# Kernel tuning notes

Measured on AMD Instinct MI355X. Metric: run time of the kernel, lower is better.

## Reference

```python
import jax, jax.numpy as jnp
import numpy as np

K_SIZE = 3
STRIDE = 1
PAD = 1


def _extract_patches(X, k, stride, pad):
    """X: [N,H,W,C] -> patches [N,Ho,Wo,k*k*C], ordered (dh, dw, c) to match
    filters.reshape(c_out, k*k*C)."""
    Xp = jnp.pad(X, ((0, 0), (pad, pad), (pad, pad), (0, 0)))
    N, Hp, Wp, C = Xp.shape
    Ho = (Hp - k) // stride + 1
    Wo = (Wp - k) // stride + 1
    slabs = [Xp[:, dh:dh + stride * Ho:stride, dw:dw + stride * Wo:stride, :]
             for dh in range(k) for dw in range(k)]  # fixed small k*k loop
    P = jnp.stack(slabs, axis=3)  # [N,Ho,Wo,k*k,C]
    return P.reshape(N, Ho, Wo, k * k * C)


def setup_inputs() -> dict:
    key = jax.random.key(0)
    k1, k2 = jax.random.split(key)
    X = jax.random.normal(k1, (8, 32, 32, 32), dtype=jnp.float32)
    filters = jax.random.normal(k2, (64, 3, 3, 32), dtype=jnp.float32)
    return {"X": X, "filters": filters}


def reference(X, filters):
    # AdderNet forward: Z[n,h,w,f] = sum_{dh,dw,c} |window(n,h,w) - filters[f]|
    c_out = filters.shape[0]
    P = _extract_patches(X, K_SIZE, STRIDE, PAD)  # [N,Ho,Wo,K]
    N, Ho, Wo, K = P.shape
    F = filters.reshape(c_out, K)
    # L1 distance between every patch and every filter: [M, c_out]
    D = jnp.abs(P.reshape(-1, 1, K) - F[None, :, :]).sum(axis=-1)
    return D.reshape(N, Ho, Wo, c_out)
```

## Files before the change

kernel.cpp:

```cpp
#include <hip/hip_runtime.h>


#define BLOCK 256

__global__ __launch_bounds__(256, 2) void adder_fwd(const float* __restrict__ X,
                                                    const float* __restrict__ Fg,
                                                    float* __restrict__ out) {
    __shared__ float Xs[4 * 34 * 36];

    const int b = blockIdx.x;
    const int fq = b & 3;
    const int hp = (b >> 2) & 15;
    const int n = b >> 6;
    const int h0 = hp * 2;
    const int tid = threadIdx.x;

    #pragma unroll
    for (int i = 0; i < 5; ++i) {
        int idx = tid + BLOCK * i;
        if (idx < 1088) {
            int c4 = idx & 7;
            int t  = idx >> 3;
            int wc = t % 34;
            int rr = t / 34;
            int hr = h0 + rr - 1;
            int gw = wc - 1;
            float4 v = make_float4(0.f, 0.f, 0.f, 0.f);
            if ((unsigned)hr < 32u && (unsigned)gw < 32u) {
                v = ((const float4*)(X + (((size_t)n * 32 + hr) * 32 + gw) * 32))[c4];
            }
            ((float4*)(Xs + (rr * 34 + wc) * 36))[c4] = v;
        }
    }
    __syncthreads();

    const int w    = tid & 31;
    const int hh   = (tid >> 5) & 1;
    const int wave = tid >> 6;
    const int f0   = fq * 16 + wave * 4;

    const float* fb = Fg + (size_t)f0 * 288;

    float a0 = 0.f, a1 = 0.f, a2 = 0.f, a3 = 0.f;

    #pragma unroll
    for (int r = 0; r < 3; ++r) {
        #pragma unroll
        for (int dw = 0; dw < 3; ++dw) {
            const float4* xp = (const float4*)(Xs + ((hh + r) * 34 + (w + dw)) * 36);
            const float*  ftap = fb + (r * 3 + dw) * 32;
            #pragma unroll
            for (int c4 = 0; c4 < 8; ++c4) {
                float4 xv = xp[c4];
                float4 f0v = ((const float4*)(ftap + 0 * 288))[c4];
                float4 f1v = ((const float4*)(ftap + 1 * 288))[c4];
                float4 f2v = ((const float4*)(ftap + 2 * 288))[c4];
                float4 f3v = ((const float4*)(ftap + 3 * 288))[c4];
                a0 += fabsf(xv.x - f0v.x) + fabsf(xv.y - f0v.y)
                    + fabsf(xv.z - f0v.z) + fabsf(xv.w - f0v.w);
                a1 += fabsf(xv.x - f1v.x) + fabsf(xv.y - f1v.y)
                    + fabsf(xv.z - f1v.z) + fabsf(xv.w - f1v.w);
                a2 += fabsf(xv.x - f2v.x) + fabsf(xv.y - f2v.y)
                    + fabsf(xv.z - f2v.z) + fabsf(xv.w - f2v.w);
                a3 += fabsf(xv.x - f3v.x) + fabsf(xv.y - f3v.y)
                    + fabsf(xv.z - f3v.z) + fabsf(xv.w - f3v.w);
            }
        }
    }

    float4* o4 = (float4*)out;
    o4[(((size_t)n * 32 + h0 + hh) * 32 + w) * 16 + (f0 >> 2)] =
        make_float4(a0, a1, a2, a3);
}

extern "C" void kernel_launch(void* const* d_in, const int* in_sizes, int n_in,
                              void* d_out, int out_size, void* d_ws, size_t ws_size,
                              hipStream_t stream) {
    const float* X = (const float*)d_in[0];
    const float* F = (const float*)d_in[1];
    float* out = (float*)d_out;
    adder_fwd<<<dim3(512), dim3(256), 0, stream>>>(X, F, out);
}
```

Measured before the change: 74.89 us.

## Pre-pad input and transpose filters, then register-tile main kernel over channels

```diff
diff --git a/kernel.cpp b/kernel.cpp
--- a/kernel.cpp
+++ b/kernel.cpp
@@ -1,76 +1,94 @@
 #include <hip/hip_runtime.h>
 
 
-#define BLOCK 256
+#define XPAD_F4 73984
+#define FT2_F4  4608
 
-__global__ __launch_bounds__(256, 2) void adder_fwd(const float* __restrict__ X,
-                                                    const float* __restrict__ Fg,
-                                                    float* __restrict__ out) {
-    __shared__ float Xs[4 * 34 * 36];
+__global__ void adder_prep(const float* __restrict__ X,
+                           const float* __restrict__ Fg,
+                           float4* __restrict__ ws) {
+    int idx = blockIdx.x * 256 + threadIdx.x;
+    if (idx < XPAD_F4) {
+        int c4 = idx & 7;
+        int t  = idx >> 3;
+        int wp = t % 34;
+        int t2 = t / 34;
+        int hp = t2 % 34;
+        int n  = t2 / 34;
+        int h = hp - 1, w = wp - 1;
+        float4 v = make_float4(0.f, 0.f, 0.f, 0.f);
+        if ((unsigned)h < 32u && (unsigned)w < 32u)
+            v = ((const float4*)X)[((n * 32 + h) * 32 + w) * 8 + c4];
+        ws[idx] = v;
+    } else if (idx < XPAD_F4 + FT2_F4) {
+        int j = idx - XPAD_F4;
+        int f   = j & 63;
+        int t3  = j >> 6;
+        int c4  = t3 & 7;
+        int tap = t3 >> 3;
+        ws[idx] = ((const float4*)Fg)[f * 72 + tap * 8 + c4];
+    }
+}
 
-    const int b = blockIdx.x;
-    const int fq = b & 3;
-    const int hp = (b >> 2) & 15;
-    const int n = b >> 6;
-    const int h0 = hp * 2;
+__global__ __launch_bounds__(512, 4) void adder_main(const float* __restrict__ ws,
+                                                     float* __restrict__ out) {
+    __shared__ float part[8 * 64 * 9];
+
+    const float*  Xpad = ws;
+    const float4* Ft2  = (const float4*)(ws + XPAD_F4 * 4);
+
+    const int b  = blockIdx.x;
+    const int wb = b & 3;
+    const int h  = (b >> 2) & 31;
+    const int n  = b >> 7;
+    const int w0 = wb * 8;
+
     const int tid = threadIdx.x;
+    const int f   = tid & 63;
+    const int c4  = __builtin_amdgcn_readfirstlane(tid >> 6);
+
+    float4 Freg[9];
+    #pragma unroll
+    for (int t = 0; t < 9; ++t)
+        Freg[t] = Ft2[(t * 8 + c4) * 64 + f];
+
+    float acc[8];
+    #pragma unroll
+    for (int w = 0; w < 8; ++w) acc[w] = 0.f;
 
     #pragma unroll
-    for (int i = 0; i < 5; ++i) {
-        int idx = tid + BLOCK * i;
-        if (idx < 1088) {
-            int c4 = idx & 7;
-            int t  = idx >> 3;
-            int wc = t % 34;
-            int rr = t / 34;
-            int hr = h0 + rr - 1;
-            int gw = wc - 1;
-            float4 v = make_float4(0.f, 0.f, 0.f, 0.f);
-            if ((unsigned)hr < 32u && (unsigned)gw < 32u) {
-                v = ((const float4*)(X + (((size_t)n * 32 + hr) * 32 + gw) * 32))[c4];
-            }
-            ((float4*)(Xs + (rr * 34 + wc) * 36))[c4] = v;
-        }
-    }
-    __syncthreads();
+    for (int dh = 0; dh < 3; ++dh) {
+        const float4* xr =
+            (const float4*)(Xpad + (((n * 34 + h + dh) * 34 + w0) * 32 + c4 * 4));
+        float4 xrow[10];
+        #pragma unroll
+        for (int k = 0; k < 10; ++k) xrow[k] = xr[k * 8];
 
-    const int w    = tid & 31;
-    const int hh   = (tid >> 5) & 1;
-    const int wave = tid >> 6;
-    const int f0   = fq * 16 + wave * 4;
-
-    const float* fb = Fg + (size_t)f0 * 288;
-
-    float a0 = 0.f, a1 = 0.f, a2 = 0.f, a3 = 0.f;
-
-    #pragma unroll
-    for (int r = 0; r < 3; ++r) {
         #pragma unroll
-        for (int dw = 0; dw < 3; ++dw) {
-            const float4* xp = (const float4*)(Xs + ((hh + r) * 34 + (w + dw)) * 36);
-            const float*  ftap = fb + (r * 3 + dw) * 32;
+        for (int w = 0; w < 8; ++w) {
             #pragma unroll
-            for (int c4 = 0; c4 < 8; ++c4) {
-                float4 xv = xp[c4];
-                float4 f0v = ((const float4*)(ftap + 0 * 288))[c4];
-                float4 f1v = ((const float4*)(ftap + 1 * 288))[c4];
-                float4 f2v = ((const float4*)(ftap + 2 * 288))[c4];
-                float4 f3v = ((const float4*)(ftap + 3 * 288))[c4];
-                a0 += fabsf(xv.x - f0v.x) + fabsf(xv.y - f0v.y)
-                    + fabsf(xv.z - f0v.z) + fabsf(xv.w - f0v.w);
-                a1 += fabsf(xv.x - f1v.x) + fabsf(xv.y - f1v.y)
-                    + fabsf(xv.z - f1v.z) + fabsf(xv.w - f1v.w);
-                a2 += fabsf(xv.x - f2v.x) + fabsf(xv.y - f2v.y)
-                    + fabsf(xv.z - f2v.z) + fabsf(xv.w - f2v.w);
-                a3 += fabsf(xv.x - f3v.x) + fabsf(xv.y - f3v.y)
-                    + fabsf(xv.z - f3v.z) + fabsf(xv.w - f3v.w);
+            for (int dw = 0; dw < 3; ++dw) {
+                float4 xv = xrow[w + dw];
+                float4 fv = Freg[dh * 3 + dw];
+                acc[w] += fabsf(xv.x - fv.x) + fabsf(xv.y - fv.y)
+                        + fabsf(xv.z - fv.z) + fabsf(xv.w - fv.w);
             }
         }
     }
 
-    float4* o4 = (float4*)out;
-    o4[(((size_t)n * 32 + h0 + hh) * 32 + w) * 16 + (f0 >> 2)] =
-        make_float4(a0, a1, a2, a3);
+    #pragma unroll
+    for (int w = 0; w < 8; ++w)
+        part[(c4 * 64 + f) * 9 + w] = acc[w];
+    __syncthreads();
+
+    const int wp = tid >> 6;
+    const int fp = tid & 63;
+    float s = 0.f;
+    #pragma unroll
+    for (int cc = 0; cc < 8; ++cc)
+        s += part[(cc * 64 + fp) * 9 + wp];
+
+    out[(((size_t)n * 32 + h) * 32 + (w0 + wp)) * 64 + fp] = s;
 }
 
 extern "C" void kernel_launch(void* const* d_in, const int* in_sizes, int n_in,
@@ -79,5 +97,8 @@
     const float* X = (const float*)d_in[0];
     const float* F = (const float*)d_in[1];
     float* out = (float*)d_out;
-    adder_fwd<<<dim3(512), dim3(256), 0, stream>>>(X, F, out);
+    float4* ws4 = (float4*)d_ws;
+
+    adder_prep<<<dim3((XPAD_F4 + FT2_F4 + 255) / 256), dim3(256), 0, stream>>>(X, F, ws4);
+    adder_main<<<dim3(1024), dim3(512), 0, stream>>>((const float*)d_ws, out);
 }
```

Result: faster. 69.89 us (-6.7%).
